# Kernel optimization log

Hardware: AMD Instinct MI355X
Metric: run time of the kernel (lower is better)

## Reference

```python
import jax, jax.numpy as jnp
import numpy as np

NUM_CODES = 8192
LATENT_DIM = 512
COMMITMENT_WEIGHT = 0.25


def l2_normalize(x, axis=-1, eps=1e-12):
    n = jnp.linalg.norm(x, axis=axis, keepdims=True)
    return x / jnp.maximum(n, eps)


def setup_inputs() -> dict:
    key = jax.random.key(0)
    k1, k2 = jax.random.split(key)
    z_e = jax.random.normal(k1, (32768, LATENT_DIM), dtype=jnp.float32)
    embeddings = jax.random.normal(k2, (NUM_CODES, LATENT_DIM), dtype=jnp.float32)
    return {"z_e": z_e, "embeddings": embeddings}


def reference(z_e, embeddings):
    B = z_e.shape[0]
    z_e_norm = l2_normalize(z_e, axis=-1)          # (B, D)
    emb_norm = l2_normalize(embeddings, axis=-1)   # (K, D)
    sim = z_e_norm @ emb_norm.T                    # (B, K) cosine similarity
    indices = jnp.argmax(sim, axis=-1)             # (B,)
    z_q = emb_norm[indices]                        # (B, D) gather

    commitment_loss = COMMITMENT_WEIGHT * jnp.mean(
        (z_e_norm - jax.lax.stop_gradient(z_q)) ** 2)
    codebook_loss = jnp.mean((jax.lax.stop_gradient(z_e_norm) - z_q) ** 2)

    # straight-through estimator
    z_q_ste = z_e_norm + jax.lax.stop_gradient(z_q - z_e_norm)

    # usage stats (one-hot mean via scatter-add)
    counts = jnp.zeros((NUM_CODES,), dtype=jnp.float32).at[indices].add(1.0)
    avg_probs = counts / B
    perplexity = jnp.exp(-jnp.sum(avg_probs * jnp.log(avg_probs + 1e-10)))
    utilization = jnp.mean((avg_probs > 0).astype(jnp.float32))

    return (z_q_ste, indices, commitment_loss, codebook_loss, perplexity,
            utilization)
```

## Files before the change

### kernel.cpp

```cpp
#include <hip/hip_runtime.h>

#define BROWS  32768
#define DDIM   512
#define NCODES 8192
#define NCHUNK 4
#define CHUNKN (NCODES / NCHUNK)
#define NSPLIT2 64
#define CHUNK2 (NCODES / NSPLIT2)
#define NF_CAP 8192
#define TM     128
#define TN     128
#define BK     32
#define NKT    (DDIM / BK)
#define MARGIN1 6.0e-4f
#define MARGIN  6e-6f

typedef unsigned short ushort_t;
typedef unsigned int   uint_t;
typedef unsigned long long ull_t;
typedef __attribute__((ext_vector_type(8))) short  short8;
typedef __attribute__((ext_vector_type(4))) float  floatx4;

__device__ __forceinline__ float wave_sum(float v) {
#pragma unroll
  for (int o = 32; o > 0; o >>= 1) v += __shfl_xor(v, o, 64);
  return v;
}

__device__ __forceinline__ floatx4 mfma16(short8 a, short8 b, floatx4 c) {
  return __builtin_amdgcn_mfma_f32_16x16x32_bf16(a, b, c, 0, 0, 0);
}

__device__ __forceinline__ void ld2lds16(const ushort_t* g, ushort_t* l) {
  __builtin_amdgcn_global_load_lds((__attribute__((address_space(1))) void*)g,
                                   (__attribute__((address_space(3))) void*)l,
                                   16, 0, 0);
}

__device__ __forceinline__ void split1(float v, ushort_t& h, ushort_t& l) {
  uint_t u  = __float_as_uint(v);
  uint_t hb = (u + 0x7FFFu + ((u >> 16) & 1u)) >> 16;
  h = (ushort_t)hb;
  float r = v - __uint_as_float(hb << 16);
  uint_t u2 = __float_as_uint(r);
  l = (ushort_t)((u2 + 0x7FFFu + ((u2 >> 16) & 1u)) >> 16);
}

__device__ __forceinline__ ull_t pack_key(float v, int c) {
  uint_t u = __float_as_uint(v);
  u = (u & 0x80000000u) ? ~u : (u | 0x80000000u);
  return ((ull_t)u << 32) | (uint_t)(NCODES - 1 - c);
}

__global__ __launch_bounds__(256) void prep_split_kernel(const float* __restrict__ x,
                                                         float* __restrict__ xn,
                                                         ushort_t* __restrict__ xh,
                                                         ushort_t* __restrict__ xl) {
  const int w = threadIdx.x >> 6, lane = threadIdx.x & 63;
  const size_t row = (size_t)blockIdx.x * 4 + w;
  const float4* src = (const float4*)(x + row * DDIM);
  float4 a = src[lane], b = src[lane + 64];
  float s = a.x*a.x + a.y*a.y + a.z*a.z + a.w*a.w
          + b.x*b.x + b.y*b.y + b.z*b.z + b.w*b.w;
  s = wave_sum(s);
  const float inv = 1.0f / fmaxf(sqrtf(s), 1e-12f);
  a.x *= inv; a.y *= inv; a.z *= inv; a.w *= inv;
  b.x *= inv; b.y *= inv; b.z *= inv; b.w *= inv;
  if (xn) {
    float4* dst = (float4*)(xn + row * DDIM);
    dst[lane] = a; dst[lane + 64] = b;
  }
  ushort4 h0, l0, h1, l1;
  split1(a.x, h0.x, l0.x); split1(a.y, h0.y, l0.y);
  split1(a.z, h0.z, l0.z); split1(a.w, h0.w, l0.w);
  split1(b.x, h1.x, l1.x); split1(b.y, h1.y, l1.y);
  split1(b.z, h1.z, l1.z); split1(b.w, h1.w, l1.w);
  ushort4* ph = (ushort4*)(xh + row * DDIM);
  ushort4* pl = (ushort4*)(xl + row * DDIM);
  ph[lane] = h0; ph[lane + 64] = h1;
  pl[lane] = l0; pl[lane + 64] = l1;
}

__device__ __forceinline__ short8 frag_read(const ushort_t* base, int off16) {
  return *(const short8*)(base + off16);
}

__global__ __launch_bounds__(256, 2) void gemm1_kernel(
    const ushort_t* __restrict__ zh, const ushort_t* __restrict__ eh,
    float* __restrict__ pv1, int* __restrict__ pi1, float* __restrict__ pv2) {
  __shared__ union {
    ushort_t stg[2][2][TM * BK];
    struct { float v1[TM][2]; float v2[TM][2]; int i1[TM][2]; } red;
  } u;
  const int t = threadIdx.x;
  const int w = t >> 6;
  const int lane = t & 63;
  const int wm = w >> 1, wn = w & 1;
  const int col = lane & 15;
  const int quad = lane >> 4;
  const int chunk = blockIdx.x;
  const int row0 = blockIdx.y * TM;

  const int swc = ((lane & 3) ^ ((lane >> 3) & 3)) * 8;
  const int matsel = w >> 1;
  const int half = w & 1;
  const ushort_t* gsrcA = zh + (size_t)(row0 + half * 64 + (lane >> 2)) * DDIM + swc;

  const int swr = (quad ^ ((col >> 1) & 3)) * 8;

  float tv1[16], tv2[16]; int ti1[16];
#pragma unroll
  for (int s = 0; s < 16; ++s) { tv1[s] = -3.0e38f; tv2[s] = -3.0e38f; ti1[s] = 0; }

  for (int ct = 0; ct < CHUNKN / TN; ++ct) {
    const int cbase = chunk * CHUNKN + ct * TN;
    const ushort_t* gsrc = (matsel == 0) ? gsrcA
        : eh + (size_t)(cbase + half * 64 + (lane >> 2)) * DDIM + swc;

    floatx4 acc[4][4];
    const floatx4 z4 = {0.f, 0.f, 0.f, 0.f};
#pragma unroll
    for (int i = 0; i < 4; ++i)
#pragma unroll
      for (int j = 0; j < 4; ++j) acc[i][j] = z4;

    {
      ushort_t* l0 = u.stg[0][matsel] + half * 2048;
#pragma unroll
      for (int i = 0; i < 4; ++i)
        ld2lds16(gsrc + (size_t)(i * 16) * DDIM, l0 + i * 512);
    }
    __syncthreads();

    for (int kt = 0; kt < NKT; ++kt) {
      const int cur = kt & 1;
      if (kt + 1 < NKT) {
        ushort_t* ln = u.stg[cur ^ 1][matsel] + half * 2048;
        const ushort_t* gn = gsrc + (kt + 1) * BK;
#pragma unroll
        for (int i = 0; i < 4; ++i)
          ld2lds16(gn + (size_t)(i * 16) * DDIM, ln + i * 512);
      }

      short8 ah[4], bh[4];
#pragma unroll
      for (int i = 0; i < 4; ++i) {
        const int offA = (wm * 64 + i * 16 + col) * BK + swr;
        const int offB = (wn * 64 + i * 16 + col) * BK + swr;
        ah[i] = frag_read(u.stg[cur][0], offA);
        bh[i] = frag_read(u.stg[cur][1], offB);
      }
#pragma unroll
      for (int i = 0; i < 4; ++i)
#pragma unroll
        for (int j = 0; j < 4; ++j)
          acc[i][j] = mfma16(ah[i], bh[j], acc[i][j]);
      __syncthreads();
    }

    int nj[4];
#pragma unroll
    for (int j = 0; j < 4; ++j) nj[j] = cbase + wn * 64 + j * 16 + col;
#pragma unroll
    for (int i = 0; i < 4; ++i)
#pragma unroll
      for (int r = 0; r < 4; ++r) {
        const int s = i * 4 + r;
#pragma unroll
        for (int j = 0; j < 4; ++j) {
          float v = acc[i][j][r];
          float mn = fminf(v, tv1[s]);
          bool gt = v > tv1[s];
          tv1[s] = gt ? v : tv1[s];
          ti1[s] = gt ? nj[j] : ti1[s];
          tv2[s] = fmaxf(tv2[s], mn);
        }
      }
  }

#pragma unroll
  for (int off = 1; off < 16; off <<= 1) {
#pragma unroll
    for (int s = 0; s < 16; ++s) {
      float ov1 = __shfl_xor(tv1[s], off, 64);
      int   oi1 = __shfl_xor(ti1[s], off, 64);
      float ov2 = __shfl_xor(tv2[s], off, 64);
      float nv2 = fmaxf(fminf(tv1[s], ov1), fmaxf(tv2[s], ov2));
      if (ov1 > tv1[s] || (ov1 == tv1[s] && oi1 < ti1[s])) { tv1[s] = ov1; ti1[s] = oi1; }
      tv2[s] = nv2;
    }
  }
  __syncthreads();
  if (col == 0) {
#pragma unroll
    for (int s = 0; s < 16; ++s) {
      const int rl = wm * 64 + (s >> 2) * 16 + quad * 4 + (s & 3);
      u.red.v1[rl][wn] = tv1[s];
      u.red.v2[rl][wn] = tv2[s];
      u.red.i1[rl][wn] = ti1[s];
    }
  }
  __syncthreads();
  if (t < TM) {
    float V1 = u.red.v1[t][0], V2 = u.red.v2[t][0];
    int   I1 = u.red.i1[t][0];
    float a1 = u.red.v1[t][1], a2 = u.red.v2[t][1];
    int   ai = u.red.i1[t][1];
    float nv2 = fmaxf(fminf(V1, a1), fmaxf(V2, a2));
    if (a1 > V1 || (a1 == V1 && ai < I1)) { V1 = a1; I1 = ai; }
    V2 = nv2;
    const size_t o = (size_t)chunk * BROWS + row0 + t;
    pv1[o] = V1; pi1[o] = I1; pv2[o] = V2;
  }
}

__global__ __launch_bounds__(256) void combine1_kernel(
    const float* __restrict__ pv1, const int* __restrict__ pi1,
    const float* __restrict__ pv2, int* __restrict__ idxs,
    int* __restrict__ flagcnt, int* __restrict__ flaglist) {
  const int row = blockIdx.x * 256 + threadIdx.x;
  float V1 = pv1[row], V2 = pv2[row];
  int I1 = pi1[row];
#pragma unroll
  for (int c2 = 1; c2 < NCHUNK; ++c2) {
    const size_t o = (size_t)c2 * BROWS + row;
    float a1 = pv1[o], a2 = pv2[o];
    int ai = pi1[o];
    float nv2 = fmaxf(fminf(V1, a1), fmaxf(V2, a2));
    if (a1 > V1) { V1 = a1; I1 = ai; }
    V2 = nv2;
  }
  idxs[row] = I1;
  if (V1 - V2 < MARGIN1) {
    int p = atomicAdd(flagcnt, 1);
    flaglist[p] = row;
  }
}

__global__ __launch_bounds__(256) void compact_kernel(
    const ushort_t* __restrict__ zh, const ushort_t* __restrict__ zl,
    const int* __restrict__ flagcnt, const int* __restrict__ flaglist,
    ushort_t* __restrict__ zhc, ushort_t* __restrict__ zlc) {
  int nf = *flagcnt;
  if (nf > NF_CAP) nf = NF_CAP;
  const int w = threadIdx.x >> 6, lane = threadIdx.x & 63;
  const int slot = blockIdx.x * 4 + w;
  if (slot >= nf) return;
  const int row = flaglist[slot];
  const float4* sh = (const float4*)(zh + (size_t)row * DDIM);
  const float4* sl = (const float4*)(zl + (size_t)row * DDIM);
  float4* dh = (float4*)(zhc + (size_t)slot * DDIM);
  float4* dl = (float4*)(zlc + (size_t)slot * DDIM);
  dh[lane] = sh[lane];
  dl[lane] = sl[lane];
}

__global__ __launch_bounds__(256, 2) void gemm3f_kernel(
    const ushort_t* __restrict__ zhc, const ushort_t* __restrict__ zlc,
    const ushort_t* __restrict__ eh, const ushort_t* __restrict__ el,
    const int* __restrict__ flagcnt,
    float* __restrict__ qv1, int* __restrict__ qi1, float* __restrict__ qv2) {
  __shared__ union {
    ushort_t stg[2][4][TM * BK];
    struct { float v1[TM][2]; float v2[TM][2]; int i1[TM][2]; } red;
  } u;
  int nf = *flagcnt;
  if (nf > NF_CAP) nf = NF_CAP;
  const int row0 = blockIdx.y * TM;
  if (row0 >= nf) return;

  const int t = threadIdx.x;
  const int w = t >> 6;
  const int lane = t & 63;
  const int wm = w >> 1, wn = w & 1;
  const int col = lane & 15;
  const int quad = lane >> 4;
  const int chunk = blockIdx.x;

  const int swc = ((lane & 3) ^ ((lane >> 3) & 3)) * 8;
  const ushort_t* eb = (w == 2) ? eh : el;
  const ushort_t* ab = (w == 0) ? zhc : zlc;
  const ushort_t* gsrcA = ab + (size_t)(row0 + (lane >> 2)) * DDIM + swc;

  const int swr = (quad ^ ((col >> 1) & 3)) * 8;

  float tv1[16], tv2[16]; int ti1[16];
#pragma unroll
  for (int s = 0; s < 16; ++s) { tv1[s] = -3.0e38f; tv2[s] = -3.0e38f; ti1[s] = 0; }

  const int cbase = chunk * CHUNK2;
  const ushort_t* gsrc = (w < 2) ? gsrcA
      : eb + (size_t)(cbase + (lane >> 2)) * DDIM + swc;

  floatx4 acc[4][4];
  const floatx4 z4 = {0.f, 0.f, 0.f, 0.f};
#pragma unroll
  for (int i = 0; i < 4; ++i)
#pragma unroll
    for (int j = 0; j < 4; ++j) acc[i][j] = z4;

  {
    ushort_t* l0 = u.stg[0][w];
#pragma unroll
    for (int i = 0; i < 8; ++i)
      ld2lds16(gsrc + (size_t)(i * 16) * DDIM, l0 + i * 512);
  }
  __syncthreads();

  for (int kt = 0; kt < NKT; ++kt) {
    const int cur = kt & 1;
    if (kt + 1 < NKT) {
      ushort_t* ln = u.stg[cur ^ 1][w];
      const ushort_t* gn = gsrc + (kt + 1) * BK;
#pragma unroll
      for (int i = 0; i < 8; ++i)
        ld2lds16(gn + (size_t)(i * 16) * DDIM, ln + i * 512);
    }

    short8 ah[4], al[4], bh[4], bl[4];
#pragma unroll
    for (int i = 0; i < 4; ++i) {
      const int offA = (wm * 64 + i * 16 + col) * BK + swr;
      const int offB = (wn * 64 + i * 16 + col) * BK + swr;
      ah[i] = frag_read(u.stg[cur][0], offA);
      al[i] = frag_read(u.stg[cur][1], offA);
      bh[i] = frag_read(u.stg[cur][2], offB);
      bl[i] = frag_read(u.stg[cur][3], offB);
    }
#pragma unroll
    for (int i = 0; i < 4; ++i)
#pragma unroll
      for (int j = 0; j < 4; ++j) {
        acc[i][j] = mfma16(ah[i], bh[j], acc[i][j]);
        acc[i][j] = mfma16(ah[i], bl[j], acc[i][j]);
        acc[i][j] = mfma16(al[i], bh[j], acc[i][j]);
      }
    __syncthreads();
  }

  int nj[4];
#pragma unroll
  for (int j = 0; j < 4; ++j) nj[j] = cbase + wn * 64 + j * 16 + col;
#pragma unroll
  for (int i = 0; i < 4; ++i)
#pragma unroll
    for (int r = 0; r < 4; ++r) {
      const int s = i * 4 + r;
#pragma unroll
      for (int j = 0; j < 4; ++j) {
        float v = acc[i][j][r];
        float mn = fminf(v, tv1[s]);
        bool gt = v > tv1[s];
        tv1[s] = gt ? v : tv1[s];
        ti1[s] = gt ? nj[j] : ti1[s];
        tv2[s] = fmaxf(tv2[s], mn);
      }
    }

#pragma unroll
  for (int off = 1; off < 16; off <<= 1) {
#pragma unroll
    for (int s = 0; s < 16; ++s) {
      float ov1 = __shfl_xor(tv1[s], off, 64);
      int   oi1 = __shfl_xor(ti1[s], off, 64);
      float ov2 = __shfl_xor(tv2[s], off, 64);
      float nv2 = fmaxf(fminf(tv1[s], ov1), fmaxf(tv2[s], ov2));
      if (ov1 > tv1[s] || (ov1 == tv1[s] && oi1 < ti1[s])) { tv1[s] = ov1; ti1[s] = oi1; }
      tv2[s] = nv2;
    }
  }
  __syncthreads();
  if (col == 0) {
#pragma unroll
    for (int s = 0; s < 16; ++s) {
      const int rl = wm * 64 + (s >> 2) * 16 + quad * 4 + (s & 3);
      u.red.v1[rl][wn] = tv1[s];
      u.red.v2[rl][wn] = tv2[s];
      u.red.i1[rl][wn] = ti1[s];
    }
  }
  __syncthreads();
  if (t < TM) {
    float V1 = u.red.v1[t][0], V2 = u.red.v2[t][0];
    int   I1 = u.red.i1[t][0];
    float a1 = u.red.v1[t][1], a2 = u.red.v2[t][1];
    int   ai = u.red.i1[t][1];
    float nv2 = fmaxf(fminf(V1, a1), fmaxf(V2, a2));
    if (a1 > V1 || (a1 == V1 && ai < I1)) { V1 = a1; I1 = ai; }
    V2 = nv2;
    const size_t o = (size_t)chunk * NF_CAP + row0 + t;
    qv1[o] = V1; qi1[o] = I1; qv2[o] = V2;
  }
}

__global__ __launch_bounds__(256) void combine2_kernel(
    const float* __restrict__ qv1, const int* __restrict__ qi1,
    const float* __restrict__ qv2, const int* __restrict__ flagcnt,
    const int* __restrict__ flaglist, int* __restrict__ idxs,
    int* __restrict__ flag2cnt, int* __restrict__ flag2list) {
  int nf = *flagcnt;
  if (nf > NF_CAP) nf = NF_CAP;
  const int f = blockIdx.x * 256 + threadIdx.x;
  if (f >= nf) return;
  float V1 = qv1[f], V2 = qv2[f];
  int I1 = qi1[f];
  for (int c2 = 1; c2 < NSPLIT2; ++c2) {
    const size_t o = (size_t)c2 * NF_CAP + f;
    float a1 = qv1[o], a2 = qv2[o];
    int ai = qi1[o];
    float nv2 = fmaxf(fminf(V1, a1), fmaxf(V2, a2));
    if (a1 > V1) { V1 = a1; I1 = ai; }
    V2 = nv2;
  }
  const int row = flaglist[f];
  idxs[row] = I1;
  if (V1 - V2 < MARGIN) {
    int p = atomicAdd(flag2cnt, 1);
    flag2list[p] = row;
  }
}

__global__ __launch_bounds__(256) void rerank_kernel(
    const float* __restrict__ z, const float* __restrict__ en,
    const int* __restrict__ flagcnt, const int* __restrict__ flaglist,
    ull_t* __restrict__ pk) {
  __shared__ float sZ[512];
  __shared__ ull_t sk[4];
  const int t = threadIdx.x;
  const int w = t >> 6, lane = t & 63;
  int nf = *flagcnt;
  if (nf > BROWS) nf = BROWS;
  const int ntask = nf * 32;
  for (int task = blockIdx.x; task < ntask; task += gridDim.x) {
    const int f = task >> 5, slab = task & 31;
    const int row = flaglist[f];
    __syncthreads();
    if (t < 128) ((float4*)sZ)[t] = ((const float4*)(z + (size_t)row * DDIM))[t];
    __syncthreads();
    const float4 za = ((const float4*)sZ)[lane];
    const float4 zb = ((const float4*)sZ)[lane + 64];
    const int c0 = slab * 256 + w * 64;
    ull_t bk = 0;
    for (int cc = 0; cc < 64; ++cc) {
      const int c = c0 + cc;
      const float4* ep = (const float4*)(en + (size_t)c * DDIM);
      float4 ea = ep[lane], eb = ep[lane + 64];
      float d = ea.x*za.x + ea.y*za.y + ea.z*za.z + ea.w*za.w
              + eb.x*zb.x + eb.y*zb.y + eb.z*zb.z + eb.w*zb.w;
      d = wave_sum(d);
      ull_t k2 = pack_key(d, c);
      if (k2 > bk) bk = k2;
    }
    if (lane == 0) sk[w] = bk;
    __syncthreads();
    if (t == 0) {
      ull_t m = sk[0];
      if (sk[1] > m) m = sk[1];
      if (sk[2] > m) m = sk[2];
      if (sk[3] > m) m = sk[3];
      atomicMax(&pk[f], m);
    }
  }
}

__global__ __launch_bounds__(256) void unpack_kernel(
    const int* __restrict__ flagcnt, const int* __restrict__ flaglist,
    const ull_t* __restrict__ pk, int* __restrict__ idxs) {
  int nf = *flagcnt;
  if (nf > BROWS) nf = BROWS;
  for (int f = blockIdx.x * 256 + threadIdx.x; f < nf; f += gridDim.x * 256)
    idxs[flaglist[f]] = (NCODES - 1) - (int)(pk[f] & 0xFFFFFFFFu);
}

__global__ __launch_bounds__(256) void finalize_kernel(const float* __restrict__ z,
                                                       const float* __restrict__ en,
                                                       const int* __restrict__ idxs,
                                                       float* __restrict__ out_q,
                                                       float* __restrict__ out_i,
                                                       float* __restrict__ counts,
                                                       float* __restrict__ lossp) {
  __shared__ float sdl[4];
  int w = threadIdx.x >> 6, lane = threadIdx.x & 63;
  int row = blockIdx.x * 4 + w;
  const float4* zr = (const float4*)(z + (size_t)row * DDIM);
  float4 a = zr[lane], b = zr[lane + 64];
  float s = a.x*a.x + a.y*a.y + a.z*a.z + a.w*a.w
          + b.x*b.x + b.y*b.y + b.z*b.z + b.w*b.w;
  s = wave_sum(s);
  float inv = 1.0f / fmaxf(sqrtf(s), 1e-12f);
  int k = idxs[row];
  const float4* qr = (const float4*)(en + (size_t)k * DDIM);
  float4 qa = qr[lane], qb = qr[lane + 64];
  float d = 0.0f;
  float4 oa, ob;
  {
    float zn;
    zn = a.x * inv; oa.x = zn + (qa.x - zn); d += (zn - qa.x) * (zn - qa.x);
    zn = a.y * inv; oa.y = zn + (qa.y - zn); d += (zn - qa.y) * (zn - qa.y);
    zn = a.z * inv; oa.z = zn + (qa.z - zn); d += (zn - qa.z) * (zn - qa.z);
    zn = a.w * inv; oa.w = zn + (qa.w - zn); d += (zn - qa.w) * (zn - qa.w);
    zn = b.x * inv; ob.x = zn + (qb.x - zn); d += (zn - qb.x) * (zn - qb.x);
    zn = b.y * inv; ob.y = zn + (qb.y - zn); d += (zn - qb.y) * (zn - qb.y);
    zn = b.z * inv; ob.z = zn + (qb.z - zn); d += (zn - qb.z) * (zn - qb.z);
    zn = b.w * inv; ob.w = zn + (qb.w - zn); d += (zn - qb.w) * (zn - qb.w);
  }
  float4* orow = (float4*)(out_q + (size_t)row * DDIM);
  orow[lane] = oa;
  orow[lane + 64] = ob;
  d = wave_sum(d);
  if (lane == 0) {
    sdl[w] = d;
    atomicAdd(&counts[k], 1.0f);
    out_i[row] = (float)k;
  }
  __syncthreads();
  if (threadIdx.x == 0)
    lossp[blockIdx.x] = sdl[0] + sdl[1] + sdl[2] + sdl[3];
}

__global__ __launch_bounds__(256) void scalars_kernel(const float* __restrict__ counts,
                                                      const float* __restrict__ lossp,
                                                      float* __restrict__ o) {
  __shared__ float se[256], su[256], sl[256];
  int t = threadIdx.x;
  float ent = 0.0f, utl = 0.0f, lsum = 0.0f;
  for (int i = t; i < NCODES; i += 256) {
    float c = counts[i];
    float p = c * (1.0f / (float)BROWS);
    ent -= p * logf(p + 1e-10f);
    utl += (c > 0.0f) ? 1.0f : 0.0f;
    lsum += lossp[i];
  }
  se[t] = ent; su[t] = utl; sl[t] = lsum;
  __syncthreads();
  for (int s2 = 128; s2 > 0; s2 >>= 1) {
    if (t < s2) { se[t] += se[t + s2]; su[t] += su[t + s2]; sl[t] += sl[t + s2]; }
    __syncthreads();
  }
  if (t == 0) {
    float mse = sl[0] * (1.0f / (float)(BROWS * DDIM));
    o[0] = 0.25f * mse;
    o[1] = mse;
    o[2] = expf(se[0]);
    o[3] = su[0] * (1.0f / (float)NCODES);
  }
}

__global__ __launch_bounds__(256) void fb_norm_rows(const float* __restrict__ e,
                                                    float* __restrict__ en) {
  int w = threadIdx.x >> 6, lane = threadIdx.x & 63;
  int row = blockIdx.x * 4 + w;
  const float4* src = (const float4*)(e + (size_t)row * DDIM);
  float4 a = src[lane], b = src[lane + 64];
  float s = a.x*a.x + a.y*a.y + a.z*a.z + a.w*a.w
          + b.x*b.x + b.y*b.y + b.z*b.z + b.w*b.w;
  s = wave_sum(s);
  float inv = 1.0f / fmaxf(sqrtf(s), 1e-12f);
  float4* dst = (float4*)(en + (size_t)row * DDIM);
  dst[lane] = make_float4(a.x*inv, a.y*inv, a.z*inv, a.w*inv);
  dst[lane + 64] = make_float4(b.x*inv, b.y*inv, b.z*inv, b.w*inv);
}

__global__ __launch_bounds__(256) void fb_gemm_argmax(const float* __restrict__ z,
                                                      const float* __restrict__ en,
                                                      int* __restrict__ out_idx) {
  __shared__ float As[16][TM + 4];
  __shared__ float Bs[16][TN + 4];
  __shared__ float rv[TM][16];
  __shared__ int   ri[TM][16];
  const int t = threadIdx.x;
  const int tx = t & 15, ty = t >> 4;
  const int row0 = blockIdx.x * TM;
  const int m = t >> 2, f4 = t & 3;
  float bestv[8]; int bestn[8];
#pragma unroll
  for (int i = 0; i < 8; ++i) { bestv[i] = -3.0e38f; bestn[i] = 0; }
  for (int ct = 0; ct < NCODES / TN; ++ct) {
    float acc[8][8];
#pragma unroll
    for (int i = 0; i < 8; ++i)
#pragma unroll
      for (int j = 0; j < 8; ++j) acc[i][j] = 0.0f;
    for (int kt = 0; kt < DDIM / 16; ++kt) {
      const int k0 = kt * 16;
      __syncthreads();
      {
        const float* zb = z + (size_t)(row0 + m) * DDIM + k0 + f4 * 4;
        float4 v0 = *(const float4*)zb;
        float4 v1 = *(const float4*)(zb + (size_t)64 * DDIM);
        const float* ebp = en + (size_t)(ct * TN + m) * DDIM + k0 + f4 * 4;
        float4 w0 = *(const float4*)ebp;
        float4 w1 = *(const float4*)(ebp + (size_t)64 * DDIM);
        const int kk = f4 * 4;
        As[kk+0][m] = v0.x; As[kk+1][m] = v0.y; As[kk+2][m] = v0.z; As[kk+3][m] = v0.w;
        As[kk+0][m+64] = v1.x; As[kk+1][m+64] = v1.y; As[kk+2][m+64] = v1.z; As[kk+3][m+64] = v1.w;
        Bs[kk+0][m] = w0.x; Bs[kk+1][m] = w0.y; Bs[kk+2][m] = w0.z; Bs[kk+3][m] = w0.w;
        Bs[kk+0][m+64] = w1.x; Bs[kk+1][m+64] = w1.y; Bs[kk+2][m+64] = w1.z; Bs[kk+3][m+64] = w1.w;
      }
      __syncthreads();
#pragma unroll
      for (int k = 0; k < 16; ++k) {
        float4 a0 = *(const float4*)&As[k][ty * 8];
        float4 a1 = *(const float4*)&As[k][ty * 8 + 4];
        float4 b0 = *(const float4*)&Bs[k][tx * 4];
        float4 b1 = *(const float4*)&Bs[k][64 + tx * 4];
        float a[8] = {a0.x,a0.y,a0.z,a0.w,a1.x,a1.y,a1.z,a1.w};
        float b[8] = {b0.x,b0.y,b0.z,b0.w,b1.x,b1.y,b1.z,b1.w};
#pragma unroll
        for (int i = 0; i < 8; ++i)
#pragma unroll
          for (int j = 0; j < 8; ++j) acc[i][j] = fmaf(a[i], b[j], acc[i][j]);
      }
    }
    const int nb = ct * TN;
#pragma unroll
    for (int i = 0; i < 8; ++i)
#pragma unroll
      for (int j = 0; j < 8; ++j) {
        int n = nb + ((j < 4) ? (tx * 4 + j) : (64 + tx * 4 + (j - 4)));
        if (acc[i][j] > bestv[i]) { bestv[i] = acc[i][j]; bestn[i] = n; }
      }
  }
#pragma unroll
  for (int i = 0; i < 8; ++i) { rv[ty*8+i][tx] = bestv[i]; ri[ty*8+i][tx] = bestn[i]; }
  __syncthreads();
  if (t < TM) {
    float bv = rv[t][0]; int bi = ri[t][0];
#pragma unroll
    for (int x = 1; x < 16; ++x) {
      float v = rv[t][x]; int n = ri[t][x];
      if (v > bv || (v == bv && n < bi)) { bv = v; bi = n; }
    }
    out_idx[row0 + t] = bi;
  }
}

extern "C" void kernel_launch(void* const* d_in, const int* in_sizes, int n_in,
                              void* d_out, int out_size, void* d_ws, size_t ws_size,
                              hipStream_t stream) {
  const float* z = (const float*)d_in[0];
  const float* e = (const float*)d_in[1];
  float* out = (float*)d_out;
  float* ws = (float*)d_ws;

  float* out_q = out;
  float* out_i = out + (size_t)BROWS * DDIM;
  float* out_s = out_i + BROWS;

  const size_t ENF = (size_t)NCODES * DDIM;
  const size_t ZNF = (size_t)BROWS * DDIM;
  const size_t NFIN = BROWS / 4;

  ushort_t* zhc = (ushort_t*)out_q;
  ushort_t* zlc = zhc + (size_t)NF_CAP * DDIM;

  size_t off = 0;
  float*    en       = ws + off;              off += ENF;
  ushort_t* enh      = (ushort_t*)(ws + off); off += ENF / 2;
  ushort_t* enl      = (ushort_t*)(ws + off); off += ENF / 2;
  ushort_t* zh       = (ushort_t*)(ws + off); off += ZNF / 2;
  ushort_t* zl       = (ushort_t*)(ws + off); off += ZNF / 2;
  float*    pv1      = ws + off;              off += (size_t)NCHUNK * BROWS;
  int*      pi1      = (int*)(ws + off);      off += (size_t)NCHUNK * BROWS;
  float*    pv2      = ws + off;              off += (size_t)NCHUNK * BROWS;
  float*    qv1      = ws + off;              off += (size_t)NSPLIT2 * NF_CAP;
  int*      qi1      = (int*)(ws + off);      off += (size_t)NSPLIT2 * NF_CAP;
  float*    qv2      = ws + off;              off += (size_t)NSPLIT2 * NF_CAP;
  int*      idxs     = (int*)(ws + off);      off += BROWS;
  int*      flaglist = (int*)(ws + off);      off += BROWS;
  int*      flag2list= (int*)(ws + off);      off += BROWS;
  float*    lossp    = ws + off;              off += NFIN;
  float*    counts   = ws + off;              off += NCODES;
  int*      flagcnt  = (int*)(ws + off);      off += 1;
  int*      flag2cnt = (int*)(ws + off);      off += 1;
  if (off & 1) off += 1;
  ull_t*    pk       = (ull_t*)(ws + off);    off += (size_t)BROWS * 2;
  const size_t need_bytes = off * sizeof(float);
  const size_t zero_bytes = (size_t)((char*)(pk + BROWS) - (char*)counts);

  if (ws_size >= need_bytes) {
    prep_split_kernel<<<NCODES / 4, 256, 0, stream>>>(e, en, enh, enl);
    prep_split_kernel<<<BROWS / 4, 256, 0, stream>>>(z, nullptr, zh, zl);
    hipMemsetAsync(counts, 0, zero_bytes, stream);
    dim3 g1(NCHUNK, BROWS / TM);
    gemm1_kernel<<<g1, 256, 0, stream>>>(zh, enh, pv1, pi1, pv2);
    combine1_kernel<<<BROWS / 256, 256, 0, stream>>>(pv1, pi1, pv2, idxs, flagcnt, flaglist);
    compact_kernel<<<NF_CAP / 4, 256, 0, stream>>>(zh, zl, flagcnt, flaglist, zhc, zlc);
    dim3 g2(NSPLIT2, NF_CAP / TM);
    gemm3f_kernel<<<g2, 256, 0, stream>>>(zhc, zlc, enh, enl, flagcnt, qv1, qi1, qv2);
    combine2_kernel<<<NF_CAP / 256, 256, 0, stream>>>(qv1, qi1, qv2, flagcnt, flaglist,
                                                      idxs, flag2cnt, flag2list);
    rerank_kernel<<<1024, 256, 0, stream>>>(z, en, flag2cnt, flag2list, pk);
    unpack_kernel<<<32, 256, 0, stream>>>(flag2cnt, flag2list, pk, idxs);
    finalize_kernel<<<BROWS / 4, 256, 0, stream>>>(z, en, idxs, out_q, out_i, counts, lossp);
    scalars_kernel<<<1, 256, 0, stream>>>(counts, lossp, out_s);
  } else {
    float* fen    = ws;
    int*   fidx   = (int*)(fen + ENF);
    float* fcnt   = (float*)(fidx + BROWS);
    float* flossp = fcnt + NCODES;
    fb_norm_rows<<<NCODES / 4, 256, 0, stream>>>(e, fen);
    hipMemsetAsync(fcnt, 0, NCODES * sizeof(float), stream);
    fb_gemm_argmax<<<BROWS / TM, 256, 0, stream>>>(z, fen, fidx);
    finalize_kernel<<<BROWS / 4, 256, 0, stream>>>(z, fen, fidx, out_q, out_i, fcnt, flossp);
    scalars_kernel<<<1, 256, 0, stream>>>(fcnt, flossp, out_s);
  }
}
```

Measured before the change: 657.8 us.

## Flatten GEMM1 loop into triple-buffered LDS pipeline with XCD-aware block mapping

Merges the code-tile and K-tile loops into one flat loop over stages. Loads now go into a three-deep LDS ring, issued two stages ahead and guarded by explicit vmcnt waits plus a bare s_barrier, so the global-to-LDS latency stays hidden across code-tile boundaries. Block IDs are also remapped so that each XCD works on a single codebook chunk, which should improve L2 reuse of the embeddings. The costs are more LDS per block, which may affect the two-blocks-per-CU occupancy, and a fragile manual waitcnt that assumes ld2lds16 issues a fixed number of loads.

```diff
diff --git a/kernel.cpp b/kernel.cpp
--- a/kernel.cpp
+++ b/kernel.cpp
@@ -12,6 +12,7 @@
 #define TN     128
 #define BK     32
 #define NKT    (DDIM / BK)
+#define NS1    ((CHUNKN / TN) * NKT)
 #define MARGIN1 6.0e-4f
 #define MARGIN  6e-6f
 
@@ -89,7 +90,7 @@
     const ushort_t* __restrict__ zh, const ushort_t* __restrict__ eh,
     float* __restrict__ pv1, int* __restrict__ pi1, float* __restrict__ pv2) {
   __shared__ union {
-    ushort_t stg[2][2][TM * BK];
+    ushort_t stg[3][2][TM * BK];
     struct { float v1[TM][2]; float v2[TM][2]; int i1[TM][2]; } red;
   } u;
   const int t = threadIdx.x;
@@ -98,13 +99,17 @@
   const int wm = w >> 1, wn = w & 1;
   const int col = lane & 15;
   const int quad = lane >> 4;
-  const int chunk = blockIdx.x;
-  const int row0 = blockIdx.y * TM;
+
+  const int lin = blockIdx.y * NCHUNK + blockIdx.x;
+  const int xcd = lin & 7, bidx = lin >> 3;
+  const int chunk = xcd >> 1;
+  const int row0 = ((xcd & 1) * 128 + bidx) * TM;
 
   const int swc = ((lane & 3) ^ ((lane >> 3) & 3)) * 8;
   const int matsel = w >> 1;
   const int half = w & 1;
   const ushort_t* gsrcA = zh + (size_t)(row0 + half * 64 + (lane >> 2)) * DDIM + swc;
+  const ushort_t* gsrcB0 = eh + (size_t)(chunk * CHUNKN + half * 64 + (lane >> 2)) * DDIM + swc;
 
   const int swr = (quad ^ ((col >> 1) & 3)) * 8;
 
@@ -112,70 +117,78 @@
 #pragma unroll
   for (int s = 0; s < 16; ++s) { tv1[s] = -3.0e38f; tv2[s] = -3.0e38f; ti1[s] = 0; }
 
-  for (int ct = 0; ct < CHUNKN / TN; ++ct) {
-    const int cbase = chunk * CHUNKN + ct * TN;
-    const ushort_t* gsrc = (matsel == 0) ? gsrcA
-        : eh + (size_t)(cbase + half * 64 + (lane >> 2)) * DDIM + swc;
-
-    floatx4 acc[4][4];
-    const floatx4 z4 = {0.f, 0.f, 0.f, 0.f};
+  floatx4 acc[4][4];
+  const floatx4 z4 = {0.f, 0.f, 0.f, 0.f};
+#pragma unroll
+  for (int i = 0; i < 4; ++i)
+#pragma unroll
+    for (int j = 0; j < 4; ++j) acc[i][j] = z4;
+
+  auto issue = [&](int s) {
+    const int ct = s >> 4, kt = s & 15;
+    const ushort_t* g = (matsel == 0)
+        ? gsrcA + (kt << 5)
+        : gsrcB0 + ((size_t)ct << 16) + (kt << 5);
+    ushort_t* l0 = u.stg[s % 3][matsel] + half * 2048;
 #pragma unroll
     for (int i = 0; i < 4; ++i)
-#pragma unroll
-      for (int j = 0; j < 4; ++j) acc[i][j] = z4;
-
-    {
-      ushort_t* l0 = u.stg[0][matsel] + half * 2048;
+      ld2lds16(g + (size_t)(i * 16) * DDIM, l0 + i * 512);
+  };
+
+  issue(0); issue(1);
+  asm volatile("s_waitcnt vmcnt(4)" ::: "memory");
+  __builtin_amdgcn_s_barrier();
+  __builtin_amdgcn_sched_barrier(0);
+
+  for (int s = 0; s < NS1; ++s) {
+    if (s + 2 < NS1) issue(s + 2);
+
+    const ushort_t* bA = u.stg[s % 3][0];
+    const ushort_t* bB = u.stg[s % 3][1];
+    short8 ah[4], bh[4];
+#pragma unroll
+    for (int i = 0; i < 4; ++i) {
+      ah[i] = frag_read(bA, (wm * 64 + i * 16 + col) * BK + swr);
+      bh[i] = frag_read(bB, (wn * 64 + i * 16 + col) * BK + swr);
+    }
+#pragma unroll
+    for (int i = 0; i < 4; ++i)
+#pragma unroll
+      for (int j = 0; j < 4; ++j)
+        acc[i][j] = mfma16(ah[i], bh[j], acc[i][j]);
+
+    if ((s & 15) == 15) {
+      const int cbase = chunk * CHUNKN + (s >> 4) * TN;
+      int nj[4];
+#pragma unroll
+      for (int j = 0; j < 4; ++j) nj[j] = cbase + wn * 64 + j * 16 + col;
 #pragma unroll
       for (int i = 0; i < 4; ++i)
-        ld2lds16(gsrc + (size_t)(i * 16) * DDIM, l0 + i * 512);
-    }
-    __syncthreads();
-
-    for (int kt = 0; kt < NKT; ++kt) {
-      const int cur = kt & 1;
-      if (kt + 1 < NKT) {
-        ushort_t* ln = u.stg[cur ^ 1][matsel] + half * 2048;
-        const ushort_t* gn = gsrc + (kt + 1) * BK;
-#pragma unroll
-        for (int i = 0; i < 4; ++i)
-          ld2lds16(gn + (size_t)(i * 16) * DDIM, ln + i * 512);
-      }
-
-      short8 ah[4], bh[4];
-#pragma unroll
-      for (int i = 0; i < 4; ++i) {
-        const int offA = (wm * 64 + i * 16 + col) * BK + swr;
-        const int offB = (wn * 64 + i * 16 + col) * BK + swr;
-        ah[i] = frag_read(u.stg[cur][0], offA);
-        bh[i] = frag_read(u.stg[cur][1], offB);
-      }
+#pragma unroll
+        for (int r = 0; r < 4; ++r) {
+          const int sv = i * 4 + r;
+#pragma unroll
+          for (int j = 0; j < 4; ++j) {
+            float v = acc[i][j][r];
+            float mn = fminf(v, tv1[sv]);
+            bool gt = v > tv1[sv];
+            tv1[sv] = gt ? v : tv1[sv];
+            ti1[sv] = gt ? nj[j] : ti1[sv];
+            tv2[sv] = fmaxf(tv2[sv], mn);
+          }
+        }
 #pragma unroll
       for (int i = 0; i < 4; ++i)
 #pragma unroll
-        for (int j = 0; j < 4; ++j)
-          acc[i][j] = mfma16(ah[i], bh[j], acc[i][j]);
-      __syncthreads();
-    }
-
-    int nj[4];
-#pragma unroll
-    for (int j = 0; j < 4; ++j) nj[j] = cbase + wn * 64 + j * 16 + col;
-#pragma unroll
-    for (int i = 0; i < 4; ++i)
-#pragma unroll
-      for (int r = 0; r < 4; ++r) {
-        const int s = i * 4 + r;
-#pragma unroll
-        for (int j = 0; j < 4; ++j) {
-          float v = acc[i][j][r];
-          float mn = fminf(v, tv1[s]);
-          bool gt = v > tv1[s];
-          tv1[s] = gt ? v : tv1[s];
-          ti1[s] = gt ? nj[j] : ti1[s];
-          tv2[s] = fmaxf(tv2[s], mn);
-        }
-      }
+        for (int j = 0; j < 4; ++j) acc[i][j] = z4;
+    }
+
+    if (s + 2 < NS1)
+      asm volatile("s_waitcnt vmcnt(4)" ::: "memory");
+    else
+      asm volatile("s_waitcnt vmcnt(0)" ::: "memory");
+    __builtin_amdgcn_s_barrier();
+    __builtin_amdgcn_sched_barrier(0);
   }
 
 #pragma unroll
```

Measured after the change: 763.5 us. +16.1%, slower.
